# Kernel tuning notes

Hardware: AMD Instinct MI355X
Metric: run time of the kernel (lower is better)

## Reference

```python
import jax, jax.numpy as jnp
import numpy as np

TPF = 36           # tokens per frame (fixed in source)
K = 4              # context frames
D = 1024           # embed_dim
H = 16             # n_heads
HD = D // H        # head_dim = 64
L = 8              # n_layers
V = 4096           # vocab_size
NA = 2             # n_actions
NL = 8             # n_levels
B = 64             # batch
S = K * (TPF + 1) + TPF   # 184


def _build_mask():
    block_idx = np.zeros(S, dtype=np.int64)
    pos = 0
    for i in range(K):
        block_idx[pos:pos + TPF] = 2 * i
        pos += TPF
        block_idx[pos] = 2 * i + 1
        pos += 1
    block_idx[pos:] = 2 * K
    mask = block_idx[:, None] < block_idx[None, :]
    ctx_end = K * (TPF + 1)
    # causal within the target frame block
    tri = np.triu(np.ones((TPF, TPF), dtype=bool), k=1)
    mask[ctx_end:ctx_end + TPF, ctx_end:ctx_end + TPF] |= tri
    return mask  # (S, S) bool, True = blocked


def _build_rope(theta=10000.0):
    freqs = 1.0 / theta ** (np.arange(0, HD, 2, dtype=np.float32) / HD)  # (HD/2,)
    t = np.arange(S, dtype=np.float32)
    ang = np.outer(t, freqs)  # (S, HD/2)
    return np.cos(ang), np.sin(ang)


def setup_inputs() -> dict:
    key = jax.random.key(0)
    ks = iter(jax.random.split(key, 40))

    def nrm(shape):
        return jax.random.normal(next(ks), shape, jnp.float32) * 0.02

    cos, sin = _build_rope()
    inp = dict(
        frame_tokens=jax.random.randint(next(ks), (B, K + 1, TPF), 0, V),
        actions=jax.random.randint(next(ks), (B, K), 0, NA),
        level_ids=jax.random.randint(next(ks), (B,), 0, NL),
        tok_emb=nrm((V, D)),
        act_emb=nrm((NA, D)),
        lvl_emb=nrm((NL, D)),
        ln1_g=jnp.ones((L, D)), ln1_b=jnp.zeros((L, D)),
        qkv_w=nrm((L, 3 * D, D)), qkv_b=jnp.zeros((L, 3 * D)),
        out_w=nrm((L, D, D)), out_b=jnp.zeros((L, D)),
        ln2_g=jnp.ones((L, D)), ln2_b=jnp.zeros((L, D)),
        mlp_w1=nrm((L, 4 * D, D)), mlp_b1=jnp.zeros((L, 4 * D)),
        mlp_w2=nrm((L, D, 4 * D)), mlp_b2=jnp.zeros((L, D)),
        lnf_g=jnp.ones((D,)), lnf_b=jnp.zeros((D,)),
        head_w=nrm((V, D)),
        death_w=nrm((1, D)), death_b=jnp.zeros((1,)),
        rope_cos=jnp.asarray(cos), rope_sin=jnp.asarray(sin),
        attn_mask=jnp.asarray(_build_mask()),
    )
    return inp


def _ln(x, g, b, eps=1e-5):
    m = x.mean(-1, keepdims=True)
    v = x.var(-1, keepdims=True)
    return (x - m) / jnp.sqrt(v + eps) * g + b


def _rope(x, cos, sin):
    # x: (B,H,T,HD); cos/sin: (T, HD/2)
    d = x.shape[-1] // 2
    x1, x2 = x[..., :d], x[..., d:]
    return jnp.concatenate([x1 * cos - x2 * sin, x1 * sin + x2 * cos], axis=-1)


def reference(frame_tokens, actions, level_ids, tok_emb, act_emb, lvl_emb,
              ln1_g, ln1_b, qkv_w, qkv_b, out_w, out_b, ln2_g, ln2_b,
              mlp_w1, mlp_b1, mlp_w2, mlp_b2, lnf_g, lnf_b,
              head_w, death_w, death_b, rope_cos, rope_sin, attn_mask):
    b = frame_tokens.shape[0]
    # interleave: [frame_i tokens (36), action_i (1)] * K, then target frame (36)
    parts = []
    for i in range(K):
        parts.append(tok_emb[frame_tokens[:, i]])          # (B, 36, D)
        parts.append(act_emb[actions[:, i]][:, None, :])   # (B, 1, D)
    parts.append(tok_emb[frame_tokens[:, K]])
    x = jnp.concatenate(parts, axis=1)                     # (B, S, D)
    x = x + lvl_emb[level_ids][:, None, :]

    scale = HD ** -0.5
    for l in range(L):
        h = _ln(x, ln1_g[l], ln1_b[l])
        qkv = h @ qkv_w[l].T + qkv_b[l]                    # (B, S, 3D)
        qkv = qkv.reshape(b, S, 3, H, HD).transpose(2, 0, 3, 1, 4)
        q, k, v = qkv[0], qkv[1], qkv[2]                   # (B, H, S, HD)
        q = _rope(q, rope_cos, rope_sin)
        k = _rope(k, rope_cos, rope_sin)
        att = jnp.einsum('bhqd,bhkd->bhqk', q, k) * scale
        att = jnp.where(attn_mask, -jnp.inf, att)
        att = jax.nn.softmax(att, axis=-1)
        h = jnp.einsum('bhqk,bhkd->bhqd', att, v)
        h = h.transpose(0, 2, 1, 3).reshape(b, S, D)
        x = x + (h @ out_w[l].T + out_b[l])
        h2 = _ln(x, ln2_g[l], ln2_b[l])
        h2 = jax.nn.gelu(h2 @ mlp_w1[l].T + mlp_b1[l], approximate=False)
        x = x + (h2 @ mlp_w2[l].T + mlp_b2[l])

    x = _ln(x, lnf_g, lnf_b)
    predict = x[:, S - TPF - 1:S - 1]                      # (B, 36, D)
    logits = predict @ head_w.T                            # (B, 36, V)
    death_logit = x[:, -1] @ death_w.T + death_b           # (B, 1)
    return logits, death_logit
```

## Files before the change

### kernel.cpp

```cpp
#include <hip/hip_runtime.h>
#include <math.h>

#define TPF 36
#define KFRM 4
#define DM 1024
#define NH 16
#define HD 64
#define NLAYER 8
#define VOCAB 4096
#define SEQ 184
#define BATCH 64
#define NTOK (BATCH * SEQ)
#define CTXEND 148

typedef unsigned short u16;
typedef unsigned int u32;
typedef __bf16 bf16x8 __attribute__((ext_vector_type(8)));
typedef float f32x4 __attribute__((ext_vector_type(4)));

struct alignas(8) U16x4 { u16 x, y, z, w; };
struct alignas(16) U16x8 { u16 v[8]; };

__device__ inline u16 f2b(float f) {
  u32 u = __float_as_uint(f);
  u += 0x7FFFu + ((u >> 16) & 1u);
  return (u16)(u >> 16);
}
__device__ inline float b2f(u16 h) { return __uint_as_float(((u32)h) << 16); }

__global__ __launch_bounds__(256) void conv_bf16(const float4* __restrict__ in,
                                                 U16x4* __restrict__ out, int n4) {
  int i = blockIdx.x * 256 + threadIdx.x;
  if (i >= n4) return;
  float4 v = in[i];
  U16x4 o;
  o.x = f2b(v.x); o.y = f2b(v.y); o.z = f2b(v.z); o.w = f2b(v.w);
  out[i] = o;
}

#define CN1 (3072 * 1024 / 4)
#define CN2 (1024 * 1024 / 4)
#define CN3 (4096 * 1024 / 4)
__global__ __launch_bounds__(256) void conv_layer(
    const float4* __restrict__ s1, U16x4* __restrict__ d1,
    const float4* __restrict__ s2, U16x4* __restrict__ d2,
    const float4* __restrict__ s3, U16x4* __restrict__ d3,
    const float4* __restrict__ s4, U16x4* __restrict__ d4) {
  int j = blockIdx.x * 256 + threadIdx.x;
  const float4* s; U16x4* d;
  if (j < CN1) { s = s1; d = d1; }
  else if ((j -= CN1) < CN2) { s = s2; d = d2; }
  else if ((j -= CN2) < CN3) { s = s3; d = d3; }
  else { j -= CN3; s = s4; d = d4; }
  float4 v = s[j];
  U16x4 o;
  o.x = f2b(v.x); o.y = f2b(v.y); o.z = f2b(v.z); o.w = f2b(v.w);
  d[j] = o;
}

__global__ __launch_bounds__(256) void embed_kernel(
    const int* __restrict__ ft, const int* __restrict__ act, const int* __restrict__ lvl,
    const float* __restrict__ tok_emb, const float* __restrict__ act_emb,
    const float* __restrict__ lvl_emb, float* __restrict__ x) {
  int row = blockIdx.x;
  int b = row / SEQ, s = row % SEQ;
  const float* src;
  if (s < CTXEND) {
    int i = s / 37, r = s % 37;
    if (r < 36) src = tok_emb + (size_t)ft[(b * 5 + i) * TPF + r] * DM;
    else        src = act_emb + (size_t)act[b * KFRM + i] * DM;
  } else {
    src = tok_emb + (size_t)ft[(b * 5 + 4) * TPF + (s - CTXEND)] * DM;
  }
  const float4* s4 = (const float4*)src;
  const float4* l4 = (const float4*)(lvl_emb + (size_t)lvl[b] * DM);
  float4* d4 = (float4*)(x + (size_t)row * DM);
  int t = threadIdx.x;
  float4 a = s4[t], l = l4[t];
  d4[t] = make_float4(a.x + l.x, a.y + l.y, a.z + l.z, a.w + l.w);
}

__global__ __launch_bounds__(256) void ln_rows(const float* __restrict__ x,
    const float* __restrict__ g, const float* __restrict__ bb,
    u16* __restrict__ out, int nrows) {
  int wid = blockIdx.x * 4 + (threadIdx.x >> 6);
  if (wid >= nrows) return;
  int lane = threadIdx.x & 63;
  const float4* row = (const float4*)(x + (size_t)wid * DM);
  float4 v[4];
  float s = 0.f, ss = 0.f;
#pragma unroll
  for (int i = 0; i < 4; i++) {
    v[i] = row[i * 64 + lane];
    s += v[i].x + v[i].y + v[i].z + v[i].w;
    ss += v[i].x * v[i].x + v[i].y * v[i].y + v[i].z * v[i].z + v[i].w * v[i].w;
  }
#pragma unroll
  for (int m = 32; m; m >>= 1) { s += __shfl_xor(s, m, 64); ss += __shfl_xor(ss, m, 64); }
  float mean = s * (1.f / DM);
  float var = ss * (1.f / DM) - mean * mean;
  float rstd = rsqrtf(var + 1e-5f);
  const float4* g4 = (const float4*)g;
  const float4* b4 = (const float4*)bb;
  U16x4* dst = (U16x4*)(out + (size_t)wid * DM);
#pragma unroll
  for (int i = 0; i < 4; i++) {
    int c = i * 64 + lane;
    float4 gg = g4[c], bbv = b4[c];
    U16x4 o;
    o.x = f2b((v[i].x - mean) * rstd * gg.x + bbv.x);
    o.y = f2b((v[i].y - mean) * rstd * gg.y + bbv.y);
    o.z = f2b((v[i].z - mean) * rstd * gg.z + bbv.z);
    o.w = f2b((v[i].w - mean) * rstd * gg.w + bbv.w);
    dst[c] = o;
  }
}

__global__ __launch_bounds__(256) void lnf_kernel(const float* __restrict__ x,
    const float* __restrict__ g, const float* __restrict__ bb,
    u16* __restrict__ pred, float* __restrict__ r183) {
  int wid = blockIdx.x * 4 + (threadIdx.x >> 6);
  if (wid >= BATCH * 37) return;
  int lane = threadIdx.x & 63;
  int b = wid / 37, si = wid % 37, s = 147 + si;
  const float4* row = (const float4*)(x + ((size_t)b * SEQ + s) * DM);
  float4 v[4];
  float sum = 0.f, ss = 0.f;
#pragma unroll
  for (int i = 0; i < 4; i++) {
    v[i] = row[i * 64 + lane];
    sum += v[i].x + v[i].y + v[i].z + v[i].w;
    ss += v[i].x * v[i].x + v[i].y * v[i].y + v[i].z * v[i].z + v[i].w * v[i].w;
  }
#pragma unroll
  for (int m = 32; m; m >>= 1) { sum += __shfl_xor(sum, m, 64); ss += __shfl_xor(ss, m, 64); }
  float mean = sum * (1.f / DM);
  float var = ss * (1.f / DM) - mean * mean;
  float rstd = rsqrtf(var + 1e-5f);
  const float4* g4 = (const float4*)g;
  const float4* b4 = (const float4*)bb;
  if (s < 183) {
    U16x4* dst = (U16x4*)(pred + ((size_t)b * 36 + si) * DM);
#pragma unroll
    for (int i = 0; i < 4; i++) {
      int c = i * 64 + lane;
      float4 gg = g4[c], bbv = b4[c];
      U16x4 o;
      o.x = f2b((v[i].x - mean) * rstd * gg.x + bbv.x);
      o.y = f2b((v[i].y - mean) * rstd * gg.y + bbv.y);
      o.z = f2b((v[i].z - mean) * rstd * gg.z + bbv.z);
      o.w = f2b((v[i].w - mean) * rstd * gg.w + bbv.w);
      dst[c] = o;
    }
  } else {
    float4* dst = (float4*)(r183 + (size_t)b * DM);
#pragma unroll
    for (int i = 0; i < 4; i++) {
      int c = i * 64 + lane;
      float4 gg = g4[c], bbv = b4[c];
      float4 o;
      o.x = (v[i].x - mean) * rstd * gg.x + bbv.x;
      o.y = (v[i].y - mean) * rstd * gg.y + bbv.y;
      o.z = (v[i].z - mean) * rstd * gg.z + bbv.z;
      o.w = (v[i].w - mean) * rstd * gg.w + bbv.w;
      dst[c] = o;
    }
  }
}

__device__ inline void gld_lds16(const void* g, void* l) {
  __builtin_amdgcn_global_load_lds((const __attribute__((address_space(1))) void*)g,
                                   (__attribute__((address_space(3))) void*)l, 16, 0, 0);
}

template <int MODE>
__global__ __launch_bounds__(1024) void gemm16(
    const u16* __restrict__ A, const u16* __restrict__ W,
    const float* __restrict__ bias, float* __restrict__ Cf, u16* __restrict__ Cb,
    int M, int Kdim) {
  __shared__ alignas(16) char As[2][32768];
  __shared__ alignas(16) char Bs[2][32768];
  const int tid = threadIdx.x;
  const int wave = tid >> 6, lane = tid & 63;
  const int wm = wave >> 2, wn = wave & 3;
  const int lr = lane & 15, g = lane >> 4;

  const int nbx = gridDim.x;
  int nwg = gridDim.x * gridDim.y;
  int id = blockIdx.y * gridDim.x + blockIdx.x;
  int id2 = (id & 7) * (nwg >> 3) + (id >> 3);
  const int row0 = (id2 / nbx) * 256, col0 = (id2 % nbx) * 256;

  const size_t krow = (size_t)Kdim * 2;
  const char* Abase = (const char*)A + (size_t)row0 * krow;
  const char* Wbase = (const char*)W + (size_t)col0 * krow;

  auto stage = [&](int t, int buf) {
    const char* Ab = Abase + (size_t)t * 128;
    const char* Wb = Wbase + (size_t)t * 128;
#pragma unroll
    for (int c = 0; c < 2; c++) {
      int ob = wave * 2048 + c * 1024;
      int o = ob + lane * 16;
      int os = o ^ (((o >> 7) & 7) << 4);
      gld_lds16(Ab + (size_t)(os >> 7) * krow + (os & 127), &As[buf][ob]);
      gld_lds16(Wb + (size_t)(os >> 7) * krow + (os & 127), &Bs[buf][ob]);
    }
  };

  const int NT = Kdim >> 6;
  f32x4 acc[4][4] = {};

  stage(0, 0);
  __syncthreads();

#pragma unroll 1
  for (int t = 0; t < NT; t++) {
    int p = t & 1;
    if (t + 1 < NT) stage(t + 1, p ^ 1);
#pragma unroll
    for (int kk = 0; kk < 2; kk++) {
      bf16x8 af[4], bfj[4];
#pragma unroll
      for (int i = 0; i < 4; i++) {
        int r = wm * 64 + i * 16 + lr;
        int o = r * 128 + kk * 64 + g * 16;
        af[i] = *(const bf16x8*)(As[p] + (o ^ ((r & 7) << 4)));
      }
#pragma unroll
      for (int j = 0; j < 4; j++) {
        int r = wn * 64 + j * 16 + lr;
        int o = r * 128 + kk * 64 + g * 16;
        bfj[j] = *(const bf16x8*)(Bs[p] + (o ^ ((r & 7) << 4)));
      }
#pragma unroll
      for (int i = 0; i < 4; i++)
#pragma unroll
        for (int j = 0; j < 4; j++)
          acc[i][j] = __builtin_amdgcn_mfma_f32_16x16x32_bf16(af[i], bfj[j], acc[i][j], 0, 0, 0);
    }
    __syncthreads();
  }

  float bj[4];
  if (MODE != 3) {
#pragma unroll
    for (int j = 0; j < 4; j++) bj[j] = bias[col0 + wn * 64 + j * 16 + lr];
  }
#pragma unroll
  for (int i = 0; i < 4; i++) {
#pragma unroll
    for (int j = 0; j < 4; j++) {
#pragma unroll
      for (int r = 0; r < 4; r++) {
        int grow = row0 + wm * 64 + i * 16 + g * 4 + r;
        int gcol = col0 + wn * 64 + j * 16 + lr;
        float v = acc[i][j][r];
        size_t idx = (size_t)grow * M + gcol;
        if (MODE == 0) { v += bj[j]; Cb[idx] = f2b(v); }
        else if (MODE == 1) { v += bj[j]; Cf[idx] += v; }
        else if (MODE == 2) {
          v += bj[j];
          float z = 1.5957692f * (v + 0.044715f * v * v * v);
          v = v / (1.f + __expf(-z));
          Cb[idx] = f2b(v);
        } else {
          Cf[idx] = v;
        }
      }
    }
  }
}

#define SP 192
#define VST 216
#define PST 216

__device__ inline int block_of(int s) {
  return (s < CTXEND) ? (2 * (s / 37) + ((s % 37) == 36)) : 8;
}

__global__ __launch_bounds__(256) void attn_mfma(const u16* __restrict__ qkv,
    u16* __restrict__ outb, const float* __restrict__ rc, const float* __restrict__ rs) {
  __shared__ alignas(16) char KsB[SP * 128];
  __shared__ alignas(16) u16 Vt[HD][VST];
  __shared__ alignas(16) u16 Ps[4][16][PST];
  const int b = blockIdx.x >> 4, h = blockIdx.x & 15;
  const int tid = threadIdx.x, wave = tid >> 6, lane = tid & 63;
  const int lr = lane & 15, g = lane >> 4, g4 = g * 4;
  const u16* base = qkv + (size_t)b * SEQ * 3072 + h * HD;

  for (int idx = tid; idx < SP * 4; idx += 256) {
    int s = idx >> 2, dq = idx & 3;
    U16x8 v0, v1;
    if (s < SEQ) {
      const u16* kr = base + (size_t)s * 3072 + 1024;
      U16x8 a = *(const U16x8*)(kr + dq * 8);
      U16x8 c8 = *(const U16x8*)(kr + 32 + dq * 8);
#pragma unroll
      for (int j = 0; j < 8; j++) {
        int d = dq * 8 + j;
        float x1 = b2f(a.v[j]), x2 = b2f(c8.v[j]);
        float c = rc[s * 32 + d], sn = rs[s * 32 + d];
        v0.v[j] = f2b(x1 * c - x2 * sn);
        v1.v[j] = f2b(x1 * sn + x2 * c);
      }
    } else {
#pragma unroll
      for (int j = 0; j < 8; j++) { v0.v[j] = 0; v1.v[j] = 0; }
    }
    *(U16x8*)(KsB + ((s * 128 + dq * 16) ^ ((s & 7) << 4))) = v0;
    *(U16x8*)(KsB + ((s * 128 + 64 + dq * 16) ^ ((s & 7) << 4))) = v1;
  }
  for (int idx = tid; idx < SP * 8; idx += 256) {
    int k = idx >> 3, d8 = (idx & 7) * 8;
    U16x8 v;
    if (k < SEQ) v = *(const U16x8*)(base + (size_t)k * 3072 + 2048 + d8);
    else {
#pragma unroll
      for (int j = 0; j < 8; j++) v.v[j] = 0;
    }
#pragma unroll
    for (int j = 0; j < 8; j++) Vt[d8 + j][k] = v.v[j];
  }
  __syncthreads();

#pragma unroll 1
  for (int t = 0; t < 3; t++) {
    const int q0 = (wave + 4 * t) * 16;
    const int q_lane = q0 + lr;
    const int qc = (q_lane < SEQ) ? q_lane : (SEQ - 1);

    U16x8 raw0 = *(const U16x8*)(base + (size_t)qc * 3072 + g * 8);
    U16x8 raw1 = *(const U16x8*)(base + (size_t)qc * 3072 + 32 + g * 8);
    bf16x8 qa0, qa1;
#pragma unroll
    for (int i = 0; i < 8; i++) {
      float x1 = b2f(raw0.v[i]), x2 = b2f(raw1.v[i]);
      int di = g * 8 + i;
      float c = rc[qc * 32 + di], sn = rs[qc * 32 + di];
      qa0[i] = (__bf16)(x1 * c - x2 * sn);
      qa1[i] = (__bf16)(x1 * sn + x2 * c);
    }

    f32x4 accs[12];
#pragma unroll
    for (int kt = 0; kt < 12; kt++) accs[kt] = (f32x4){0.f, 0.f, 0.f, 0.f};
#pragma unroll
    for (int kt = 0; kt < 12; kt++) {
      int rt = kt * 16 + lr;
      bf16x8 kb0 = *(const bf16x8*)(KsB + ((rt * 128 + g * 16) ^ ((rt & 7) << 4)));
      bf16x8 kb1 = *(const bf16x8*)(KsB + ((rt * 128 + 64 + g * 16) ^ ((rt & 7) << 4)));
      accs[kt] = __builtin_amdgcn_mfma_f32_16x16x32_bf16(qa0, kb0, accs[kt], 0, 0, 0);
      accs[kt] = __builtin_amdgcn_mfma_f32_16x16x32_bf16(qa1, kb1, accs[kt], 0, 0, 0);
    }

    int qb[4];
#pragma unroll
    for (int r = 0; r < 4; r++) qb[r] = block_of(q0 + g4 + r);
    float mr[4] = {-3e38f, -3e38f, -3e38f, -3e38f};
#pragma unroll
    for (int kt = 0; kt < 12; kt++) {
      int k = kt * 16 + lr;
      bool kv = k < SEQ;
      int kb = kv ? block_of(k) : 9;
#pragma unroll
      for (int r = 0; r < 4; r++) {
        int q = q0 + g4 + r;
        bool ok = kv && (kb <= qb[r]) && !(q >= CTXEND && k >= CTXEND && k > q);
        float s = ok ? accs[kt][r] * 0.125f : -3e38f;
        accs[kt][r] = s;
        mr[r] = fmaxf(mr[r], s);
      }
    }
#pragma unroll
    for (int m = 1; m <= 8; m <<= 1)
#pragma unroll
      for (int r = 0; r < 4; r++) mr[r] = fmaxf(mr[r], __shfl_xor(mr[r], m, 64));

    float sr[4] = {0.f, 0.f, 0.f, 0.f};
#pragma unroll
    for (int kt = 0; kt < 12; kt++) {
#pragma unroll
      for (int r = 0; r < 4; r++) {
        float e = (accs[kt][r] > -1e37f) ? __expf(accs[kt][r] - mr[r]) : 0.f;
        Ps[wave][g4 + r][kt * 16 + lr] = f2b(e);
        sr[r] += e;
      }
    }
#pragma unroll
    for (int m = 1; m <= 8; m <<= 1)
#pragma unroll
      for (int r = 0; r < 4; r++) sr[r] += __shfl_xor(sr[r], m, 64);
    float inv[4];
#pragma unroll
    for (int r = 0; r < 4; r++) inv[r] = 1.f / sr[r];

    __builtin_amdgcn_s_waitcnt(0);

    f32x4 acco[4];
#pragma unroll
    for (int dt = 0; dt < 4; dt++) acco[dt] = (f32x4){0.f, 0.f, 0.f, 0.f};
#pragma unroll
    for (int kc = 0; kc < 6; kc++) {
      bf16x8 pa = *(const bf16x8*)&Ps[wave][lr][kc * 32 + g * 8];
#pragma unroll
      for (int dt = 0; dt < 4; dt++) {
        bf16x8 vb = *(const bf16x8*)&Vt[dt * 16 + lr][kc * 32 + g * 8];
        acco[dt] = __builtin_amdgcn_mfma_f32_16x16x32_bf16(pa, vb, acco[dt], 0, 0, 0);
      }
    }

#pragma unroll
    for (int dt = 0; dt < 4; dt++) {
#pragma unroll
      for (int r = 0; r < 4; r++) {
        int q = q0 + g4 + r;
        if (q < SEQ)
          outb[((size_t)b * SEQ + q) * DM + h * HD + dt * 16 + lr] = f2b(acco[dt][r] * inv[r]);
      }
    }
  }
}

__global__ void death_kernel(const float* __restrict__ r183, const float* __restrict__ dw,
                             const float* __restrict__ db, float* __restrict__ out) {
  int b = blockIdx.x, lane = threadIdx.x;
  const float4* r4 = (const float4*)(r183 + (size_t)b * DM);
  const float4* w4 = (const float4*)dw;
  float a = 0.f;
#pragma unroll
  for (int i = 0; i < 4; i++) {
    float4 rv = r4[i * 64 + lane], wv = w4[i * 64 + lane];
    a += rv.x * wv.x + rv.y * wv.y + rv.z * wv.z + rv.w * wv.w;
  }
#pragma unroll
  for (int m = 32; m; m >>= 1) a += __shfl_xor(a, m, 64);
  if (lane == 0) out[(size_t)BATCH * TPF * VOCAB + b] = a + db[0];
}

extern "C" void kernel_launch(void* const* d_in, const int* in_sizes, int n_in,
                              void* d_out, int out_size, void* d_ws, size_t ws_size,
                              hipStream_t stream) {
  const int* ft = (const int*)d_in[0];
  const int* act = (const int*)d_in[1];
  const int* lvl = (const int*)d_in[2];
  const float* tok_emb = (const float*)d_in[3];
  const float* act_emb = (const float*)d_in[4];
  const float* lvl_emb = (const float*)d_in[5];
  const float* ln1_g = (const float*)d_in[6];
  const float* ln1_b = (const float*)d_in[7];
  const float* qkv_w = (const float*)d_in[8];
  const float* qkv_b = (const float*)d_in[9];
  const float* out_w = (const float*)d_in[10];
  const float* out_b = (const float*)d_in[11];
  const float* ln2_g = (const float*)d_in[12];
  const float* ln2_b = (const float*)d_in[13];
  const float* mlp_w1 = (const float*)d_in[14];
  const float* mlp_b1 = (const float*)d_in[15];
  const float* mlp_w2 = (const float*)d_in[16];
  const float* mlp_b2 = (const float*)d_in[17];
  const float* lnf_g = (const float*)d_in[18];
  const float* lnf_b = (const float*)d_in[19];
  const float* head_w = (const float*)d_in[20];
  const float* death_w = (const float*)d_in[21];
  const float* death_b = (const float*)d_in[22];
  const float* rope_cos = (const float*)d_in[23];
  const float* rope_sin = (const float*)d_in[24];

  char* ws = (char*)d_ws;
  size_t off = 0;
  auto alloc = [&](size_t bytes) {
    void* p = ws + off;
    off += (bytes + 255) & ~(size_t)255;
    return p;
  };
  float* x   = (float*)alloc((size_t)NTOK * DM * 4);
  u16* hb    = (u16*)alloc((size_t)NTOK * DM * 2);
  u16* big   = (u16*)alloc((size_t)NTOK * 4096 * 2);
  u16* wq    = (u16*)alloc((size_t)3072 * 1024 * 2);
  u16* wo    = (u16*)alloc((size_t)1024 * 1024 * 2);
  u16* w1    = (u16*)alloc((size_t)4096 * 1024 * 2);
  u16* w2    = (u16*)alloc((size_t)4096 * 1024 * 2);
  u16* pred  = (u16*)alloc((size_t)BATCH * 36 * DM * 2);
  float* r183 = (float*)alloc((size_t)BATCH * DM * 4);

  float* out = (float*)d_out;

  embed_kernel<<<NTOK, 256, 0, stream>>>(ft, act, lvl, tok_emb, act_emb, lvl_emb, x);

  for (int l = 0; l < NLAYER; l++) {
    conv_layer<<<(CN1 + CN2 + 2 * CN3) / 256, 256, 0, stream>>>(
        (const float4*)(qkv_w + (size_t)l * 3072 * 1024), (U16x4*)wq,
        (const float4*)(out_w + (size_t)l * 1024 * 1024), (U16x4*)wo,
        (const float4*)(mlp_w1 + (size_t)l * 4096 * 1024), (U16x4*)w1,
        (const float4*)(mlp_w2 + (size_t)l * 4096 * 1024), (U16x4*)w2);

    ln_rows<<<NTOK / 4, 256, 0, stream>>>(x, ln1_g + l * DM, ln1_b + l * DM, hb, NTOK);
    gemm16<0><<<dim3(3072 / 256, NTOK / 256), 1024, 0, stream>>>(
        hb, wq, qkv_b + (size_t)l * 3072, nullptr, big, 3072, 1024);
    attn_mfma<<<BATCH * NH, 256, 0, stream>>>(big, hb, rope_cos, rope_sin);
    gemm16<1><<<dim3(1024 / 256, NTOK / 256), 1024, 0, stream>>>(
        hb, wo, out_b + (size_t)l * DM, x, nullptr, 1024, 1024);
    ln_rows<<<NTOK / 4, 256, 0, stream>>>(x, ln2_g + l * DM, ln2_b + l * DM, hb, NTOK);
    gemm16<2><<<dim3(4096 / 256, NTOK / 256), 1024, 0, stream>>>(
        hb, w1, mlp_b1 + (size_t)l * 4096, nullptr, big, 4096, 1024);
    gemm16<1><<<dim3(1024 / 256, NTOK / 256), 1024, 0, stream>>>(
        big, w2, mlp_b2 + (size_t)l * DM, x, nullptr, 1024, 4096);
  }

  lnf_kernel<<<BATCH * 37 / 4, 256, 0, stream>>>(x, lnf_g, lnf_b, pred, r183);
  conv_bf16<<<4096 * 1024 / 4 / 256, 256, 0, stream>>>(
      (const float4*)head_w, (U16x4*)w1, 4096 * 1024 / 4);
  gemm16<3><<<dim3(4096 / 256, BATCH * 36 / 256), 1024, 0, stream>>>(
      pred, w1, nullptr, out, nullptr, 4096, 1024);
  death_kernel<<<BATCH, 64, 0, stream>>>(r183, death_w, death_b, out);
}
```

Measured before the change: 3.606 ms.

## Use four-stage LDS ring with BK=32 and prefetch distance two in GEMM

The GEMM main loop is restructured from a double-buffered 64-wide K tile to a four-slot ring of 32-wide K tiles, issuing global-to-LDS loads two steps ahead. Manual s_waitcnt vmcnt plus s_barrier replace __syncthreads so that only the oldest stage is waited on, which keeps more loads in flight and is meant to hide memory latency better. The swizzle changes to fit the 64-byte rows. The trade-off is twice as many barriers per K, less MFMA work between syncs, and a reliance on inline-asm wait counts being correct.

```diff
diff --git a/kernel.cpp b/kernel.cpp
--- a/kernel.cpp
+++ b/kernel.cpp
@@ -178,8 +178,8 @@
     const u16* __restrict__ A, const u16* __restrict__ W,
     const float* __restrict__ bias, float* __restrict__ Cf, u16* __restrict__ Cb,
     int M, int Kdim) {
-  __shared__ alignas(16) char As[2][32768];
-  __shared__ alignas(16) char Bs[2][32768];
+  __shared__ alignas(16) char As[4][16384];
+  __shared__ alignas(16) char Bs[4][16384];
   const int tid = threadIdx.x;
   const int wave = tid >> 6, lane = tid & 63;
   const int wm = wave >> 2, wn = wave & 3;
@@ -192,54 +192,51 @@
   const int row0 = (id2 / nbx) * 256, col0 = (id2 % nbx) * 256;
 
   const size_t krow = (size_t)Kdim * 2;
-  const char* Abase = (const char*)A + (size_t)row0 * krow;
-  const char* Wbase = (const char*)W + (size_t)col0 * krow;
-
-  auto stage = [&](int t, int buf) {
-    const char* Ab = Abase + (size_t)t * 128;
-    const char* Wb = Wbase + (size_t)t * 128;
-#pragma unroll
-    for (int c = 0; c < 2; c++) {
-      int ob = wave * 2048 + c * 1024;
-      int o = ob + lane * 16;
-      int os = o ^ (((o >> 7) & 7) << 4);
-      gld_lds16(Ab + (size_t)(os >> 7) * krow + (os & 127), &As[buf][ob]);
-      gld_lds16(Wb + (size_t)(os >> 7) * krow + (os & 127), &Bs[buf][ob]);
-    }
-  };
-
-  const int NT = Kdim >> 6;
+
+  const int o16 = tid * 16;
+  const int os = o16 ^ (((o16 >> 6) & 3) << 4);
+  const char* srcA = (const char*)A + (size_t)(row0 + (os >> 6)) * krow + (os & 63);
+  const char* srcB = (const char*)W + (size_t)(col0 + (os >> 6)) * krow + (os & 63);
+
+  const int NT = Kdim >> 5;
   f32x4 acc[4][4] = {};
 
-  stage(0, 0);
-  __syncthreads();
+  gld_lds16(srcA, &As[0][o16]); gld_lds16(srcB, &Bs[0][o16]); srcA += 64; srcB += 64;
+  gld_lds16(srcA, &As[1][o16]); gld_lds16(srcB, &Bs[1][o16]); srcA += 64; srcB += 64;
+  asm volatile("s_waitcnt vmcnt(2)" ::: "memory");
+  asm volatile("s_barrier" ::: "memory");
 
 #pragma unroll 1
   for (int t = 0; t < NT; t++) {
-    int p = t & 1;
-    if (t + 1 < NT) stage(t + 1, p ^ 1);
-#pragma unroll
-    for (int kk = 0; kk < 2; kk++) {
-      bf16x8 af[4], bfj[4];
-#pragma unroll
-      for (int i = 0; i < 4; i++) {
-        int r = wm * 64 + i * 16 + lr;
-        int o = r * 128 + kk * 64 + g * 16;
-        af[i] = *(const bf16x8*)(As[p] + (o ^ ((r & 7) << 4)));
-      }
-#pragma unroll
-      for (int j = 0; j < 4; j++) {
-        int r = wn * 64 + j * 16 + lr;
-        int o = r * 128 + kk * 64 + g * 16;
-        bfj[j] = *(const bf16x8*)(Bs[p] + (o ^ ((r & 7) << 4)));
-      }
-#pragma unroll
-      for (int i = 0; i < 4; i++)
-#pragma unroll
-        for (int j = 0; j < 4; j++)
-          acc[i][j] = __builtin_amdgcn_mfma_f32_16x16x32_bf16(af[i], bfj[j], acc[i][j], 0, 0, 0);
-    }
-    __syncthreads();
+    int s = t & 3;
+    if (t + 2 < NT) {
+      int sn = (t + 2) & 3;
+      gld_lds16(srcA, &As[sn][o16]); gld_lds16(srcB, &Bs[sn][o16]);
+      srcA += 64; srcB += 64;
+    }
+    bf16x8 af[4], bfj[4];
+#pragma unroll
+    for (int i = 0; i < 4; i++) {
+      int r = wm * 64 + i * 16 + lr;
+      int o = (r * 64 + g * 16) ^ ((r & 3) << 4);
+      af[i] = *(const bf16x8*)(As[s] + o);
+    }
+#pragma unroll
+    for (int j = 0; j < 4; j++) {
+      int r = wn * 64 + j * 16 + lr;
+      int o = (r * 64 + g * 16) ^ ((r & 3) << 4);
+      bfj[j] = *(const bf16x8*)(Bs[s] + o);
+    }
+#pragma unroll
+    for (int i = 0; i < 4; i++)
+#pragma unroll
+      for (int j = 0; j < 4; j++)
+        acc[i][j] = __builtin_amdgcn_mfma_f32_16x16x32_bf16(af[i], bfj[j], acc[i][j], 0, 0, 0);
+    if (t + 1 < NT) {
+      if (t + 2 < NT) { asm volatile("s_waitcnt vmcnt(2)" ::: "memory"); }
+      else            { asm volatile("s_waitcnt vmcnt(0)" ::: "memory"); }
+      asm volatile("s_barrier" ::: "memory");
+    }
   }
 
   float bj[4];
```

Measured after the change: 4.267 ms. 18.3% more time.
